# Performance work log

Hardware: AMD Instinct MI355X
Metric: run time of the kernel (lower is better)

Reference implementation:

```python
import jax, jax.numpy as jnp
import numpy as np

D_BERT, D_LSTM, T, B = 768, 512, 256, 32
H = D_LSTM // 2  # per-direction hidden
X = 10           # additive attention hidden width


def setup_inputs() -> dict:
    key = jax.random.key(0)
    ks = jax.random.split(key, 12)
    s = lambda fan: 1.0 / np.sqrt(fan)
    u = lambda k, shape, fan: jax.random.uniform(k, shape, jnp.float32, -s(fan), s(fan))
    return {
        "x": jax.random.normal(ks[0], (B, T, D_BERT), jnp.float32),
        "mask": jnp.ones((B, T), jnp.float32),
        # forward-direction LSTM params (torch gate order i,f,g,o)
        "Wih_f": u(ks[1], (4 * H, D_BERT), H),
        "Whh_f": u(ks[2], (4 * H, H), H),
        "b_f": u(ks[3], (4 * H,), H),  # b_ih + b_hh fused
        # backward-direction LSTM params
        "Wih_b": u(ks[4], (4 * H, D_BERT), H),
        "Whh_b": u(ks[5], (4 * H, H), H),
        "b_b": u(ks[6], (4 * H,), H),
        # attention MLP: fc1 [X, 2*D_LSTM] no bias, fc2 [1, X] no bias, fc3 [D_LSTM, 2*D_LSTM] + bias
        "W1": u(ks[7], (X, 2 * D_LSTM), 2 * D_LSTM),
        "W2": u(ks[8], (1, X), X),
        "W3": u(ks[9], (D_LSTM, 2 * D_LSTM), 2 * D_LSTM),
        "b3": u(ks[10], (D_LSTM,), 2 * D_LSTM),
    }


def _lstm_dir(x_btd, Wih, Whh, b):
    """Single-direction LSTM over [B,T,D]; returns hidden states [B,T,H]."""
    Bc = x_btd.shape[0]
    h0 = jnp.zeros((Bc, H), x_btd.dtype)
    c0 = jnp.zeros((Bc, H), x_btd.dtype)
    # precompute input projections for all timesteps: [T,B,4H]
    xz = jnp.einsum('btd,gd->tbg', x_btd, Wih) + b

    def step(carry, xzt):
        h, c = carry
        z = xzt + h @ Whh.T
        i, f, g, o = jnp.split(z, 4, axis=-1)
        i, f, o = jax.nn.sigmoid(i), jax.nn.sigmoid(f), jax.nn.sigmoid(o)
        c = f * c + i * jnp.tanh(g)
        h = o * jnp.tanh(c)
        return (h, c), h

    _, hs = jax.lax.scan(step, (h0, c0), xz)
    return jnp.swapaxes(hs, 0, 1)  # [B,T,H]


def reference(x, mask, Wih_f, Whh_f, b_f, Wih_b, Whh_b, b_b, W1, W2, W3, b3):
    # Bidirectional LSTM: forward + reversed backward pass, concat on features
    hf = _lstm_dir(x, Wih_f, Whh_f, b_f)
    hb = _lstm_dir(x[:, ::-1], Wih_b, Whh_b, b_b)[:, ::-1]
    h = jnp.concatenate([hf, hb], axis=-1)  # [B,T,D_LSTM]

    # Additive attention. fc1 has no bias, so fc1(cat(q,k)) = q@W1q.T + k@W1k.T;
    # compute per-token projections then broadcast-add -> only [B,T,T,X] materialized.
    W1q, W1k = W1[:, :D_LSTM], W1[:, D_LSTM:]
    sq = jnp.einsum('btd,xd->btx', h, W1q)  # query proj [B,T,X]
    sk = jnp.einsum('btd,xd->btx', h, W1k)  # key proj   [B,T,X]
    a = jnp.einsum('bqkx,x->bqk', jnp.tanh(sq[:, :, None, :] + sk[:, None, :, :]), W2[0])

    madd = jnp.where(mask == 0, -jnp.inf, 0.0)[:, None, :]  # [B,1,T]
    w = jax.nn.softmax(a + madd, axis=-1)                   # [B,T,T]
    context = jnp.einsum('bqk,bkd->bqd', w, h)              # [B,T,D_LSTM]

    y = jnp.concatenate([h, context], axis=-1) @ W3.T + b3  # [B,T,D_LSTM]
    return y
```

## Files before the change

### kernel.cpp

```cpp
#include <hip/hip_runtime.h>
#include <stdint.h>

#define B_   32
#define T_   256
#define H_   256
#define DB_  768
#define DL_  512

#define OFF_DTYPE 0u
#define OFF_FLAGS 256u
#define OFF_HBUF  4096u
#define OFF_XZ    69632u
#define XZ_DIR_ELEMS 8388608u
#define NEED_CONC (OFF_XZ + 2u*16777216u + 8388608u)
#define OFF_CTX   OFF_XZ
#define OFF_WATT  (OFF_XZ + 8388608u)
#define OFF_SQ    (OFF_XZ + 12582912u)
#define OFF_SK    (OFF_SQ + 327680u)

typedef __attribute__((ext_vector_type(8))) short bf16x8;
typedef __attribute__((ext_vector_type(4))) float f32x4;
typedef __attribute__((ext_vector_type(4))) uint32_t u32x4;
typedef unsigned short ushort_t;

__device__ __forceinline__ float b2f(ushort_t u){ union{float f; uint32_t i;} v; v.i=((uint32_t)u)<<16; return v.f; }
__device__ __forceinline__ ushort_t f2b(float f){
  union{float ff; uint32_t i;} v; v.ff=f;
  uint32_t r = v.i + 0x7fffu + ((v.i>>16)&1u);
  return (ushort_t)(r>>16);
}
__device__ __forceinline__ float sig_f(float x){ return 1.f/(1.f+__expf(-x)); }
__device__ __forceinline__ float tanh_f(float x){ return 1.f - 2.f/(1.f+__expf(2.f*x)); }

__device__ __forceinline__ bf16x8 load8(const ushort_t* p, size_t idx, int isbf){
  if (isbf) return *(const bf16x8*)(p + idx);
  const float* f = (const float*)p;
  bf16x8 r;
  #pragma unroll
  for (int i=0;i<8;++i) r[i] = (short)f2b(f[idx+i]);
  return r;
}
__device__ __forceinline__ float loadS(const ushort_t* p, size_t idx, int isbf){
  return isbf ? b2f(p[idx]) : ((const float*)p)[idx];
}

__global__ void detect_k(const uint32_t* __restrict__ x, char* __restrict__ ws){
  __shared__ int cnt;
  if (threadIdx.x == 0) cnt = 0;
  __syncthreads();
  int local = 0;
  #pragma unroll
  for (int i=0;i<4;++i){
    uint32_t w = x[threadIdx.x*4 + i];
    uint32_t lo = w & 0xFFFFu;
    int e = (int)((lo >> 7) & 0xFFu);
    if (e >= 118 && e <= 130) local++;
  }
  atomicAdd(&cnt, local);
  __syncthreads();
  if (threadIdx.x == 0) *(int*)(ws + OFF_DTYPE) = (cnt > 512) ? 1 : 0;
}

template<int MODE>
__global__ __launch_bounds__(256,2) void gemm_k(
    const ushort_t* __restrict__ A0, const ushort_t* __restrict__ A2,
    const ushort_t* __restrict__ Bm, const ushort_t* __restrict__ bias,
    ushort_t* __restrict__ Cout, char* __restrict__ ws,
    int lda, int ldb, int K, int dir, int aIn, int bIn,
    long aOffZ, long bOffZ, long cOffZ)
{
  __shared__ ushort_t As[8192];
  __shared__ ushort_t Bs[8192];
  const int dtf = *(const int*)(ws + OFF_DTYPE);
  const int aBF = aIn ? dtf : 1;
  const int bBF = bIn ? dtf : 1;
  const int tid = threadIdx.x;
  const int l  = tid & 63, wv = tid >> 6;
  const int lc = l & 15,  lh = l >> 4;
  const int m0 = blockIdx.x * 128, n0 = blockIdx.y * 128;
  const int z  = blockIdx.z;
  const ushort_t* Abase = A0 + (size_t)z * aOffZ;
  const ushort_t* Bbase = Bm + (size_t)z * bOffZ;
  const int srow = tid >> 3;
  const int sch  = tid & 7;

  f32x4 acc[4][4];
  #pragma unroll
  for (int i=0;i<4;++i)
    #pragma unroll
    for (int j=0;j<4;++j) acc[i][j] = (f32x4){0.f,0.f,0.f,0.f};

  bf16x8 ra[4], rb[4];
  #pragma unroll
  for (int p=0;p<4;++p){
    int row = p*32 + srow;
    int kk  = (sch ^ (row & 7)) * 8;
    ra[p] = load8(Abase, (size_t)(m0+row)*lda + kk, aBF);
    if (MODE==3){
      int q = p*256 + tid, kr = q>>4, c = q&15;
      rb[p] = load8(Bbase, (size_t)kr*ldb + n0 + c*8, 1);
    } else {
      rb[p] = load8(Bbase, (size_t)(n0+row)*ldb + kk, bBF);
    }
  }

  const int mo = (wv&1)*64, no = (wv>>1)*64;

  for (int k0 = 0; k0 < K; k0 += 64) {
    #pragma unroll
    for (int p=0;p<4;++p){
      int row = p*32 + srow;
      *(bf16x8*)(&As[row*64 + sch*8]) = ra[p];
      if (MODE==3){
        int q = p*256 + tid, kr = q>>4, c = q&15;
        *(bf16x8*)(&Bs[kr*128 + c*8]) = rb[p];
      } else {
        *(bf16x8*)(&Bs[row*64 + sch*8]) = rb[p];
      }
    }
    __syncthreads();
    int k1 = k0 + 64;
    if (k1 < K) {
      #pragma unroll
      for (int p=0;p<4;++p){
        int row = p*32 + srow;
        int kk  = k1 + (sch ^ (row & 7)) * 8;
        if (MODE==2 && k1 >= 512)
          ra[p] = load8(A2, (size_t)(m0+row)*512 + (kk - 512), 1);
        else
          ra[p] = load8(Abase, (size_t)(m0+row)*lda + kk, aBF);
        if (MODE==3){
          int q = p*256 + tid, kr = q>>4, c = q&15;
          rb[p] = load8(Bbase, (size_t)(k1+kr)*ldb + n0 + c*8, 1);
        } else {
          rb[p] = load8(Bbase, (size_t)(n0+row)*ldb + kk, bBF);
        }
      }
    }
    #pragma unroll
    for (int kc=0;kc<2;++kc){
      bf16x8 af[4], bfv[4];
      #pragma unroll
      for (int it=0;it<4;++it){
        int m = mo + it*16 + lc;
        int gc = kc*4 + lh;
        af[it]  = *(const bf16x8*)(&As[m*64 + ((gc ^ (m&7))*8)]);
        int n = no + it*16 + lc;
        if (MODE==3){
          #pragma unroll
          for (int j=0;j<8;++j) bfv[it][j] = (short)Bs[(kc*32 + lh*8 + j)*128 + n];
        } else {
          bfv[it] = *(const bf16x8*)(&Bs[n*64 + ((gc ^ (n&7))*8)]);
        }
      }
      #pragma unroll
      for (int mt=0;mt<4;++mt)
        #pragma unroll
        for (int nt=0;nt<4;++nt)
          acc[mt][nt] = __builtin_amdgcn_mfma_f32_16x16x32_bf16(af[mt], bfv[nt], acc[mt][nt], 0,0,0);
    }
    __syncthreads();
  }

  ushort_t* xzsw = (ushort_t*)(ws + OFF_XZ);
  #pragma unroll
  for (int mt=0;mt<4;++mt){
    #pragma unroll
    for (int nt=0;nt<4;++nt){
      #pragma unroll
      for (int r=0;r<4;++r){
        int m = m0 + mo + mt*16 + lh*4 + r;
        int n = n0 + no + nt*16 + lc;
        float v = acc[mt][nt][r];
        if (MODE==0){
          v += loadS(bias, n, bBF);
          int b = m >> 8, t = m & 255;
          int ts = dir ? (255 - t) : t;
          int q = n >> 8, jm = n & 255;
          int w = jm >> 6, jj = jm & 63, wvv = jj >> 4, colj = jj & 15;
          int lane = ((b >> 2) & 3)*16 + colj;
          int idx  = (b >> 4)*16 + q*4 + (b & 3);
          size_t e = (((size_t)(w*4 + wvv)*256 + ts)*2048) + (size_t)lane*32 + idx;
          xzsw[e + (size_t)cOffZ] = f2b(v);
        } else if (MODE==3){
          Cout[(size_t)z*cOffZ + (size_t)m*DL_ + n] = f2b(v);
        } else {
          v += loadS(bias, n, bBF);
          if (dtf) Cout[(size_t)m*DL_ + n] = f2b(v);
          else     ((float*)Cout)[(size_t)m*DL_ + n] = v;
        }
      }
    }
  }
}

__global__ __launch_bounds__(256,1) void rec_k(
    const ushort_t* __restrict__ Whh_f, const ushort_t* __restrict__ Whh_b,
    char* __restrict__ ws, ushort_t* __restrict__ hist,
    int dParam, long xzDirStride)
{
  __shared__ ushort_t wlds[32768];
  const int d  = (gridDim.x == 16) ? (int)(blockIdx.x >> 3) : dParam;
  const int bw = (int)(blockIdx.x & 7);
  const int tid = threadIdx.x;
  const int wv = tid >> 6, l = tid & 63;
  const int lc = l & 15, lh = l >> 4;
  const int bh = wv & 1, hh = wv >> 1;
  const int dtf = *(const int*)(ws + OFF_DTYPE);

  uint32_t* flags = (uint32_t*)(ws + OFF_FLAGS);
  uint32_t* hbuf  = (uint32_t*)(ws + OFF_HBUF);
  const ushort_t* xz = (const ushort_t*)(ws + OFF_XZ) + (size_t)d * xzDirStride;
  const ushort_t* Whh = d ? Whh_b : Whh_f;

  const int jj = bw*32 + hh*16 + lc;
  const int g  = bw*2 + hh;

  #pragma unroll
  for (int i=0;i<16;++i){
    int f   = wv*16 + i;
    int fhh = f >> 5, fnt = (f >> 3) & 3, fkc = f & 7;
    int row = fnt*256 + bw*32 + fhh*16 + lc;
    bf16x8 v = load8(Whh, (size_t)row*256 + fkc*32 + lh*8, dtf);
    *(bf16x8*)(&wlds[f*512 + l*8]) = v;
  }
  __syncthreads();
  const int wbase = (hh*4)*8;

  float cst[4] = {0.f, 0.f, 0.f, 0.f};

  const ushort_t* xzb = xz + (size_t)g*256*2048 + (size_t)l*32 + bh*16;
  const int hOffByte = (bh*16 + lc)*512 + lh*16;

  for (int t=0; t<T_; ++t){
    bf16x8 xzv[2];
    xzv[0] = *(const bf16x8*)(xzb + (size_t)t*2048);
    xzv[1] = *(const bf16x8*)(xzb + (size_t)t*2048 + 8);

    f32x4 acc[4];
    #pragma unroll
    for (int j=0;j<4;++j) acc[j] = (f32x4){0.f,0.f,0.f,0.f};

    if (t > 0){
      if (tid == 0){
        const uint32_t* fl = flags + d*T_ + (t-1);
        while (__hip_atomic_load(fl, __ATOMIC_RELAXED, __HIP_MEMORY_SCOPE_AGENT) < 8u) {}
      }
      __syncthreads();

      const uint32_t* hb = hbuf + (size_t)(((t-1)&1)*2 + d)*(B_*H_/2);
      __amdgpu_buffer_rsrc_t rs =
        __builtin_amdgcn_make_buffer_rsrc((void*)hb, (short)0, 0xFFFFFFFFu, 0x00020000);
      u32x4 hreg[8];
      #pragma unroll
      for (int kc=0;kc<8;++kc)
        hreg[kc] = __builtin_bit_cast(u32x4,
          __builtin_amdgcn_raw_buffer_load_b128(rs, hOffByte + kc*64, 0, 17));

      #pragma unroll
      for (int kc=0;kc<8;++kc){
        bf16x8 a = __builtin_bit_cast(bf16x8, hreg[kc]);
        #pragma unroll
        for (int nt=0;nt<4;++nt){
          bf16x8 wfrag = *(const bf16x8*)(&wlds[(wbase + nt*8 + kc)*512 + l*8]);
          acc[nt] = __builtin_amdgcn_mfma_f32_16x16x32_bf16(a, wfrag, acc[nt], 0,0,0);
        }
      }
    }

    const int ts = d ? (255 - t) : t;
    uint32_t* hb_out = hbuf + (size_t)((t&1)*2 + d)*(B_*H_/2);
    uint32_t* histw  = (uint32_t*)hist;
    #pragma unroll
    for (int r=0;r<4;++r){
      float zi = acc[0][r] + b2f((ushort_t)xzv[(r+0 )>>3][(r+0 )&7]);
      float zf = acc[1][r] + b2f((ushort_t)xzv[(r+4 )>>3][(r+4 )&7]);
      float zg = acc[2][r] + b2f((ushort_t)xzv[(r+8 )>>3][(r+8 )&7]);
      float zo = acc[3][r] + b2f((ushort_t)xzv[(r+12)>>3][(r+12)&7]);
      float ig = sig_f(zi), fg = sig_f(zf), gg = tanh_f(zg), og = sig_f(zo);
      float c = fg * cst[r] + ig * gg;
      cst[r] = c;
      float h = og * tanh_f(c);
      ushort_t h16 = f2b(h);
      int b = bh*16 + lh*4 + r;
      uint32_t mine = (uint32_t)h16;
      uint32_t partner = (uint32_t)__shfl_xor((int)mine, 1);
      if ((lc & 1) == 0){
        uint32_t packed = mine | (partner << 16);
        __hip_atomic_store(hb_out + (size_t)b*128 + (jj>>1), packed,
                           __ATOMIC_RELAXED, __HIP_MEMORY_SCOPE_AGENT);
        histw[(((size_t)(b*256 + ts))*512 + d*256 + jj) >> 1] = packed;
      }
    }
    __builtin_amdgcn_s_waitcnt(0);
    __syncthreads();
    if (tid == 0)
      __hip_atomic_fetch_add(flags + d*T_ + t, 1u, __ATOMIC_RELAXED, __HIP_MEMORY_SCOPE_AGENT);
  }
}

__global__ __launch_bounds__(256) void c1_k(char* __restrict__ ws, const ushort_t* __restrict__ W1,
                                            const ushort_t* __restrict__ hist)
{
  float* sq = (float*)(ws + OFF_SQ);
  float* sk = (float*)(ws + OFF_SK);
  const int dtf = *(const int*)(ws + OFF_DTYPE);
  int tid = threadIdx.x; int wv = tid>>6, l = tid&63;
  int row = blockIdx.x*4 + wv;
  bf16x8 hv = *(const bf16x8*)(hist + (size_t)row*512 + l*8);
  float hf[8];
  #pragma unroll
  for (int i=0;i<8;++i) hf[i] = b2f((ushort_t)hv[i]);
  #pragma unroll
  for (int x=0;x<10;++x){
    bf16x8 qv = load8(W1, (size_t)x*1024 + l*8, dtf);
    bf16x8 kv = load8(W1, (size_t)x*1024 + 512 + l*8, dtf);
    float pq=0.f, pk=0.f;
    #pragma unroll
    for (int i=0;i<8;++i){ pq += hf[i]*b2f((ushort_t)qv[i]); pk += hf[i]*b2f((ushort_t)kv[i]); }
    #pragma unroll
    for (int off=32; off>0; off>>=1){ pq += __shfl_xor(pq, off, 64); pk += __shfl_xor(pk, off, 64); }
    if (l == 0){ sq[row*10 + x] = pq; sk[row*10 + x] = pk; }
  }
}

__global__ __launch_bounds__(256) void c2_k(char* __restrict__ ws, const ushort_t* __restrict__ W2,
                                            const ushort_t* __restrict__ mask)
{
  const float* sq = (const float*)(ws + OFF_SQ);
  const float* sk = (const float*)(ws + OFF_SK);
  ushort_t* watt = (ushort_t*)(ws + OFF_WATT);
  const int dtf = *(const int*)(ws + OFF_DTYPE);
  int tid = threadIdx.x; int wv = tid>>6, l = tid&63;
  int bq = blockIdx.x*4 + wv;
  int b  = bq >> 8;
  float sqv[10], w2v[10];
  #pragma unroll
  for (int x=0;x<10;++x){ sqv[x] = sq[(size_t)bq*10+x]; w2v[x] = loadS(W2, x, dtf); }
  float a[4];
  #pragma unroll
  for (int kk=0;kk<4;++kk){
    int k = kk*64 + l;
    const float* skp = sk + ((size_t)b*256 + k)*10;
    float s = 0.f;
    #pragma unroll
    for (int x=0;x<10;++x) s += tanh_f(sqv[x] + skp[x]) * w2v[x];
    float mval = loadS(mask, (size_t)b*256 + k, dtf);
    a[kk] = (mval == 0.f) ? -1e30f : s;
  }
  float mx = fmaxf(fmaxf(a[0],a[1]), fmaxf(a[2],a[3]));
  #pragma unroll
  for (int off=32; off>0; off>>=1) mx = fmaxf(mx, __shfl_xor(mx, off, 64));
  float e[4], ssum=0.f;
  #pragma unroll
  for (int kk=0;kk<4;++kk){ e[kk] = __expf(a[kk]-mx); ssum += e[kk]; }
  #pragma unroll
  for (int off=32; off>0; off>>=1) ssum += __shfl_xor(ssum, off, 64);
  float inv = 1.f/ssum;
  #pragma unroll
  for (int kk=0;kk<4;++kk) watt[(size_t)bq*256 + kk*64 + l] = f2b(e[kk]*inv);
}

extern "C" void kernel_launch(void* const* d_in, const int* in_sizes, int n_in,
                              void* d_out, int out_size, void* d_ws, size_t ws_size,
                              hipStream_t stream)
{
  const ushort_t* x     = (const ushort_t*)d_in[0];
  const ushort_t* mask  = (const ushort_t*)d_in[1];
  const ushort_t* Wih_f = (const ushort_t*)d_in[2];
  const ushort_t* Whh_f = (const ushort_t*)d_in[3];
  const ushort_t* b_f   = (const ushort_t*)d_in[4];
  const ushort_t* Wih_b = (const ushort_t*)d_in[5];
  const ushort_t* Whh_b = (const ushort_t*)d_in[6];
  const ushort_t* b_b   = (const ushort_t*)d_in[7];
  const ushort_t* W1    = (const ushort_t*)d_in[8];
  const ushort_t* W2    = (const ushort_t*)d_in[9];
  const ushort_t* W3    = (const ushort_t*)d_in[10];
  const ushort_t* b3    = (const ushort_t*)d_in[11];
  ushort_t* out = (ushort_t*)d_out;
  char* ws = (char*)d_ws;

  const bool conc = ws_size >= (size_t)NEED_CONC;
  ushort_t* hist = (ushort_t*)(ws + OFF_XZ + (conc ? 33554432u : 16777216u));

  hipMemsetAsync(ws, 0, 4096, stream);
  detect_k<<<dim3(1), dim3(256), 0, stream>>>((const uint32_t*)d_in[0], ws);

  dim3 blk(256);
  if (conc){
    gemm_k<0><<<dim3(64,8,1), blk, 0, stream>>>(x, nullptr, Wih_f, b_f, nullptr, ws,
                                                DB_, DB_, DB_, 0, 1, 1, 0,0, 0L);
    gemm_k<0><<<dim3(64,8,1), blk, 0, stream>>>(x, nullptr, Wih_b, b_b, nullptr, ws,
                                                DB_, DB_, DB_, 1, 1, 1, 0,0, (long)XZ_DIR_ELEMS);
    rec_k<<<dim3(16), blk, 0, stream>>>(Whh_f, Whh_b, ws, hist, 0, (long)XZ_DIR_ELEMS);
  } else {
    gemm_k<0><<<dim3(64,8,1), blk, 0, stream>>>(x, nullptr, Wih_f, b_f, nullptr, ws,
                                                DB_, DB_, DB_, 0, 1, 1, 0,0, 0L);
    rec_k<<<dim3(8), blk, 0, stream>>>(Whh_f, Whh_b, ws, hist, 0, 0L);
    gemm_k<0><<<dim3(64,8,1), blk, 0, stream>>>(x, nullptr, Wih_b, b_b, nullptr, ws,
                                                DB_, DB_, DB_, 1, 1, 1, 0,0, 0L);
    rec_k<<<dim3(8), blk, 0, stream>>>(Whh_f, Whh_b, ws, hist, 1, 0L);
  }
  c1_k<<<dim3(2048), blk, 0, stream>>>(ws, W1, hist);
  c2_k<<<dim3(2048), blk, 0, stream>>>(ws, W2, mask);
  gemm_k<3><<<dim3(2,4,32), blk, 0, stream>>>((ushort_t*)(ws+OFF_WATT), nullptr,
                                              hist, nullptr,
                                              (ushort_t*)(ws+OFF_CTX), ws,
                                              256, 512, 256, 0, 0, 0,
                                              65536L, 131072L, 131072L);
  gemm_k<2><<<dim3(64,4,1), blk, 0, stream>>>(hist, (ushort_t*)(ws+OFF_CTX),
                                              W3, b3, out, ws,
                                              512, 1024, 1024, 0, 0, 1, 0,0, 0L);
}
```

Before: 1.356 ms.

## Use per-block step flags and add spinning filler blocks to recurrence kernel

The single shared step counter, polled by one thread and followed by __syncthreads, is replaced with per-block slots. Each block stores its completed step, and every thread polls all eight slots directly, which removes the barrier after the wait and the atomic increments from the serial LSTM loop. The recurrence launch is also padded with extra blocks that spin on FMA work until the real blocks set a done flag. The likely aim is to keep the device busy so clocks stay high during the latency-bound recurrence. This burns power and CUs, and it relies on the real blocks being scheduled before the filler blocks.

```diff
diff --git a/kernel.cpp b/kernel.cpp
--- a/kernel.cpp
+++ b/kernel.cpp
@@ -9,6 +9,7 @@
 
 #define OFF_DTYPE 0u
 #define OFF_FLAGS 256u
+#define OFF_DONE  512u
 #define OFF_HBUF  4096u
 #define OFF_XZ    69632u
 #define XZ_DIR_ELEMS 8388608u
@@ -197,18 +198,41 @@
 __global__ __launch_bounds__(256,1) void rec_k(
     const ushort_t* __restrict__ Whh_f, const ushort_t* __restrict__ Whh_b,
     char* __restrict__ ws, ushort_t* __restrict__ hist,
-    int dParam, long xzDirStride)
+    int dParam, long xzDirStride, int nReal)
 {
   __shared__ ushort_t wlds[32768];
-  const int d  = (gridDim.x == 16) ? (int)(blockIdx.x >> 3) : dParam;
-  const int bw = (int)(blockIdx.x & 7);
+  const int bid = (int)blockIdx.x;
   const int tid = threadIdx.x;
+  uint32_t* done = (uint32_t*)(ws + OFF_DONE);
+
+  if (bid >= nReal) {
+    const uint32_t needMask = (nReal == 16) ? 3u : (1u << dParam);
+    float a = 1.0f + (float)tid * 1e-3f, b = 2.0f, c = 3.0f, e = 4.0f;
+    for (;;) {
+      uint32_t g0 = __hip_atomic_load(done + 0, __ATOMIC_RELAXED, __HIP_MEMORY_SCOPE_AGENT);
+      uint32_t g1 = __hip_atomic_load(done + 1, __ATOMIC_RELAXED, __HIP_MEMORY_SCOPE_AGENT);
+      uint32_t got = (g0 ? 1u : 0u) | (g1 ? 2u : 0u);
+      if ((got & needMask) == needMask) break;
+      #pragma unroll
+      for (int i = 0; i < 256; ++i) {
+        a = __builtin_fmaf(a, 1.0000001f, 1e-7f);
+        b = __builtin_fmaf(b, 0.9999999f, 1e-7f);
+        c = __builtin_fmaf(c, 1.0000002f, 1e-7f);
+        e = __builtin_fmaf(e, 0.9999998f, 1e-7f);
+      }
+      asm volatile("" : "+v"(a), "+v"(b), "+v"(c), "+v"(e));
+    }
+    return;
+  }
+
+  const int d  = (nReal == 16) ? (bid >> 3) : dParam;
+  const int bw = bid & 7;
   const int wv = tid >> 6, l = tid & 63;
   const int lc = l & 15, lh = l >> 4;
   const int bh = wv & 1, hh = wv >> 1;
   const int dtf = *(const int*)(ws + OFF_DTYPE);
 
-  uint32_t* flags = (uint32_t*)(ws + OFF_FLAGS);
+  uint32_t* frow  = (uint32_t*)(ws + OFF_FLAGS + (size_t)d * 128);
   uint32_t* hbuf  = (uint32_t*)(ws + OFF_HBUF);
   const ushort_t* xz = (const ushort_t*)(ws + OFF_XZ) + (size_t)d * xzDirStride;
   const ushort_t* Whh = d ? Whh_b : Whh_f;
@@ -242,11 +266,24 @@
     for (int j=0;j<4;++j) acc[j] = (f32x4){0.f,0.f,0.f,0.f};
 
     if (t > 0){
-      if (tid == 0){
-        const uint32_t* fl = flags + d*T_ + (t-1);
-        while (__hip_atomic_load(fl, __ATOMIC_RELAXED, __HIP_MEMORY_SCOPE_AGENT) < 8u) {}
-      }
-      __syncthreads();
+      const uint32_t tv = (uint32_t)t;
+      for (;;){
+        uint32_t f0 = __hip_atomic_load(frow+0, __ATOMIC_RELAXED, __HIP_MEMORY_SCOPE_AGENT);
+        uint32_t f1 = __hip_atomic_load(frow+1, __ATOMIC_RELAXED, __HIP_MEMORY_SCOPE_AGENT);
+        uint32_t f2 = __hip_atomic_load(frow+2, __ATOMIC_RELAXED, __HIP_MEMORY_SCOPE_AGENT);
+        uint32_t f3 = __hip_atomic_load(frow+3, __ATOMIC_RELAXED, __HIP_MEMORY_SCOPE_AGENT);
+        uint32_t f4 = __hip_atomic_load(frow+4, __ATOMIC_RELAXED, __HIP_MEMORY_SCOPE_AGENT);
+        uint32_t f5 = __hip_atomic_load(frow+5, __ATOMIC_RELAXED, __HIP_MEMORY_SCOPE_AGENT);
+        uint32_t f6 = __hip_atomic_load(frow+6, __ATOMIC_RELAXED, __HIP_MEMORY_SCOPE_AGENT);
+        uint32_t f7 = __hip_atomic_load(frow+7, __ATOMIC_RELAXED, __HIP_MEMORY_SCOPE_AGENT);
+        uint32_t m0 = f0 < f1 ? f0 : f1;
+        uint32_t m1 = f2 < f3 ? f2 : f3;
+        uint32_t m2 = f4 < f5 ? f4 : f5;
+        uint32_t m3 = f6 < f7 ? f6 : f7;
+        uint32_t ma = m0 < m1 ? m0 : m1;
+        uint32_t mb = m2 < m3 ? m2 : m3;
+        if ((ma < mb ? ma : mb) >= tv) break;
+      }
 
       const uint32_t* hb = hbuf + (size_t)(((t-1)&1)*2 + d)*(B_*H_/2);
       __amdgpu_buffer_rsrc_t rs =
@@ -295,8 +332,12 @@
     __builtin_amdgcn_s_waitcnt(0);
     __syncthreads();
     if (tid == 0)
-      __hip_atomic_fetch_add(flags + d*T_ + t, 1u, __ATOMIC_RELAXED, __HIP_MEMORY_SCOPE_AGENT);
-  }
+      __hip_atomic_store(frow + bw, (uint32_t)(t+1),
+                         __ATOMIC_RELAXED, __HIP_MEMORY_SCOPE_AGENT);
+  }
+
+  if (tid == 0 && bw == 0)
+    __hip_atomic_store(done + d, 1u, __ATOMIC_RELAXED, __HIP_MEMORY_SCOPE_AGENT);
 }
 
 __global__ __launch_bounds__(256) void c1_k(char* __restrict__ ws, const ushort_t* __restrict__ W1,
@@ -392,14 +433,14 @@
                                                 DB_, DB_, DB_, 0, 1, 1, 0,0, 0L);
     gemm_k<0><<<dim3(64,8,1), blk, 0, stream>>>(x, nullptr, Wih_b, b_b, nullptr, ws,
                                                 DB_, DB_, DB_, 1, 1, 1, 0,0, (long)XZ_DIR_ELEMS);
-    rec_k<<<dim3(16), blk, 0, stream>>>(Whh_f, Whh_b, ws, hist, 0, (long)XZ_DIR_ELEMS);
+    rec_k<<<dim3(256), blk, 0, stream>>>(Whh_f, Whh_b, ws, hist, 0, (long)XZ_DIR_ELEMS, 16);
   } else {
     gemm_k<0><<<dim3(64,8,1), blk, 0, stream>>>(x, nullptr, Wih_f, b_f, nullptr, ws,
                                                 DB_, DB_, DB_, 0, 1, 1, 0,0, 0L);
-    rec_k<<<dim3(8), blk, 0, stream>>>(Whh_f, Whh_b, ws, hist, 0, 0L);
+    rec_k<<<dim3(248), blk, 0, stream>>>(Whh_f, Whh_b, ws, hist, 0, 0L, 8);
     gemm_k<0><<<dim3(64,8,1), blk, 0, stream>>>(x, nullptr, Wih_b, b_b, nullptr, ws,
                                                 DB_, DB_, DB_, 1, 1, 1, 0,0, 0L);
-    rec_k<<<dim3(8), blk, 0, stream>>>(Whh_f, Whh_b, ws, hist, 1, 0L);
+    rec_k<<<dim3(248), blk, 0, stream>>>(Whh_f, Whh_b, ws, hist, 1, 0L, 8);
   }
   c1_k<<<dim3(2048), blk, 0, stream>>>(ws, W1, hist);
   c2_k<<<dim3(2048), blk, 0, stream>>>(ws, W2, mask);
```

Result: no change. 1.362 ms (+0.5%).

## Replace flag-based step barrier with sentinel polling on history buffer

Applied to the files above, without the earlier changes.

The recurrent kernel no longer waits on per-step counters and a block-wide barrier. Each wave now polls the history buffer directly until no word still holds a sentinel value, which is pre-filled with a memset. The hidden state is written once, atomically, into the history buffer, which drops the separate double-buffered exchange. The aim is lower per-timestep latency on the serial LSTM chain, at the cost of an extra 8MB memset and repeated reloads while spinning. Correctness depends on bf16 outputs never equalling the 0x7F7F pattern.

```diff
diff --git a/kernel.cpp b/kernel.cpp
--- a/kernel.cpp
+++ b/kernel.cpp
@@ -8,8 +8,6 @@
 #define DL_  512
 
 #define OFF_DTYPE 0u
-#define OFF_FLAGS 256u
-#define OFF_HBUF  4096u
 #define OFF_XZ    69632u
 #define XZ_DIR_ELEMS 8388608u
 #define NEED_CONC (OFF_XZ + 2u*16777216u + 8388608u)
@@ -17,6 +15,8 @@
 #define OFF_WATT  (OFF_XZ + 8388608u)
 #define OFF_SQ    (OFF_XZ + 12582912u)
 #define OFF_SK    (OFF_SQ + 327680u)
+
+#define SENTINEL 0x7F7F7F7Fu
 
 typedef __attribute__((ext_vector_type(8))) short bf16x8;
 typedef __attribute__((ext_vector_type(4))) float f32x4;
@@ -208,8 +208,6 @@
   const int bh = wv & 1, hh = wv >> 1;
   const int dtf = *(const int*)(ws + OFF_DTYPE);
 
-  uint32_t* flags = (uint32_t*)(ws + OFF_FLAGS);
-  uint32_t* hbuf  = (uint32_t*)(ws + OFF_HBUF);
   const ushort_t* xz = (const ushort_t*)(ws + OFF_XZ) + (size_t)d * xzDirStride;
   const ushort_t* Whh = d ? Whh_b : Whh_f;
 
@@ -230,7 +228,12 @@
   float cst[4] = {0.f, 0.f, 0.f, 0.f};
 
   const ushort_t* xzb = xz + (size_t)g*256*2048 + (size_t)l*32 + bh*16;
-  const int hOffByte = (bh*16 + lc)*512 + lh*16;
+  const int bb = bh*16 + lc;
+  const uint32_t hOffBase = (uint32_t)bb*262144u + (uint32_t)d*512u + (uint32_t)lh*16u;
+
+  __amdgpu_buffer_rsrc_t hrs =
+    __builtin_amdgcn_make_buffer_rsrc((void*)hist, (short)0, 0xFFFFFFFFu, 0x00020000);
+  uint32_t* histw = (uint32_t*)hist;
 
   for (int t=0; t<T_; ++t){
     bf16x8 xzv[2];
@@ -242,20 +245,26 @@
     for (int j=0;j<4;++j) acc[j] = (f32x4){0.f,0.f,0.f,0.f};
 
     if (t > 0){
-      if (tid == 0){
-        const uint32_t* fl = flags + d*T_ + (t-1);
-        while (__hip_atomic_load(fl, __ATOMIC_RELAXED, __HIP_MEMORY_SCOPE_AGENT) < 8u) {}
-      }
-      __syncthreads();
-
-      const uint32_t* hb = hbuf + (size_t)(((t-1)&1)*2 + d)*(B_*H_/2);
-      __amdgpu_buffer_rsrc_t rs =
-        __builtin_amdgcn_make_buffer_rsrc((void*)hb, (short)0, 0xFFFFFFFFu, 0x00020000);
+      const int tsp = d ? (256 - t) : (t - 1);
+      const uint32_t off0 = hOffBase + (uint32_t)tsp*1024u;
       u32x4 hreg[8];
-      #pragma unroll
-      for (int kc=0;kc<8;++kc)
-        hreg[kc] = __builtin_bit_cast(u32x4,
-          __builtin_amdgcn_raw_buffer_load_b128(rs, hOffByte + kc*64, 0, 17));
+      for (;;){
+        asm volatile("" ::: "memory");
+        #pragma unroll
+        for (int kc=0;kc<8;++kc)
+          hreg[kc] = __builtin_bit_cast(u32x4,
+            __builtin_amdgcn_raw_buffer_load_b128(hrs, off0 + kc*64, 0, 17));
+        int ok = 1;
+        #pragma unroll
+        for (int kc=0;kc<8;++kc){
+          ok &= (hreg[kc][0] != SENTINEL);
+          ok &= (hreg[kc][1] != SENTINEL);
+          ok &= (hreg[kc][2] != SENTINEL);
+          ok &= (hreg[kc][3] != SENTINEL);
+        }
+        if (__all(ok)) break;
+      }
+      asm volatile("" ::: "memory");
 
       #pragma unroll
       for (int kc=0;kc<8;++kc){
@@ -269,8 +278,6 @@
     }
 
     const int ts = d ? (255 - t) : t;
-    uint32_t* hb_out = hbuf + (size_t)((t&1)*2 + d)*(B_*H_/2);
-    uint32_t* histw  = (uint32_t*)hist;
     #pragma unroll
     for (int r=0;r<4;++r){
       float zi = acc[0][r] + b2f((ushort_t)xzv[(r+0 )>>3][(r+0 )&7]);
@@ -282,20 +289,15 @@
       cst[r] = c;
       float h = og * tanh_f(c);
       ushort_t h16 = f2b(h);
-      int b = bh*16 + lh*4 + r;
       uint32_t mine = (uint32_t)h16;
       uint32_t partner = (uint32_t)__shfl_xor((int)mine, 1);
       if ((lc & 1) == 0){
+        int b = bh*16 + lh*4 + r;
         uint32_t packed = mine | (partner << 16);
-        __hip_atomic_store(hb_out + (size_t)b*128 + (jj>>1), packed,
-                           __ATOMIC_RELAXED, __HIP_MEMORY_SCOPE_AGENT);
-        histw[(((size_t)(b*256 + ts))*512 + d*256 + jj) >> 1] = packed;
-      }
-    }
-    __builtin_amdgcn_s_waitcnt(0);
-    __syncthreads();
-    if (tid == 0)
-      __hip_atomic_fetch_add(flags + d*T_ + t, 1u, __ATOMIC_RELAXED, __HIP_MEMORY_SCOPE_AGENT);
+        __hip_atomic_store(histw + (size_t)(b*256 + ts)*256 + (size_t)(d*128 + (jj>>1)),
+                           packed, __ATOMIC_RELAXED, __HIP_MEMORY_SCOPE_AGENT);
+      }
+    }
   }
 }
 
@@ -384,6 +386,7 @@
   ushort_t* hist = (ushort_t*)(ws + OFF_XZ + (conc ? 33554432u : 16777216u));
 
   hipMemsetAsync(ws, 0, 4096, stream);
+  hipMemsetAsync(hist, 0x7F, 8388608, stream);
   detect_k<<<dim3(1), dim3(256), 0, stream>>>((const uint32_t*)d_in[0], ws);
 
   dim3 blk(256);
```

Result: slower. 1.449 ms (+6.9%).
